# Kernel tuning notes

Hardware: AMD Instinct MI355X
Metric: run time of the kernel (lower is better)

## Reference

```python
import jax, jax.numpy as jnp
import numpy as np

N_NODES = 30000
N_EDGES = 300000
N_GRAPHS = 512
SEQ = 1000
HEADS = 10
CH = 78


def setup_inputs() -> dict:
    key = jax.random.key(0)
    ks = jax.random.split(key, 20)
    def w(k, shape, scale=0.02):
        return jax.random.normal(k, shape, jnp.float32) * scale
    x = jax.random.normal(ks[0], (N_NODES, CH), jnp.float32)
    edge_index = jax.random.randint(ks[1], (2, N_EDGES), 0, N_NODES, jnp.int32)
    # every graph gets a contiguous block of nodes (sorted batch vector)
    batch = (jnp.arange(N_NODES) * N_GRAPHS // N_NODES).astype(jnp.int32)
    target = jax.random.randint(ks[2], (N_GRAPHS, SEQ), 0, 26, jnp.int32)
    return {
        "x": x, "edge_index": edge_index, "batch": batch, "target": target,
        "W_gat": w(ks[3], (CH, HEADS * CH)),
        "att_src": w(ks[4], (HEADS, CH), 0.1),
        "att_dst": w(ks[5], (HEADS, CH), 0.1),
        "b_gat": jnp.zeros((HEADS * CH,), jnp.float32),
        "W_gcn": w(ks[6], (HEADS * CH, HEADS * CH)),
        "b_gcn": jnp.zeros((HEADS * CH,), jnp.float32),
        "W_fcg1": w(ks[7], (2 * HEADS * CH, 1500)), "b_fcg1": jnp.zeros((1500,), jnp.float32),
        "W_fcg2": w(ks[8], (1500, 128)), "b_fcg2": jnp.zeros((128,), jnp.float32),
        "emb": w(ks[9], (26, 128), 1.0),
        "W_conv": w(ks[10], (32, 1000, 8)), "b_conv": jnp.zeros((32,), jnp.float32),
        "W_fcxt": w(ks[11], (32 * 121, 128)), "b_fcxt": jnp.zeros((128,), jnp.float32),
        "W_fc1": w(ks[12], (256, 1024)), "b_fc1": jnp.zeros((1024,), jnp.float32),
        "W_fc2": w(ks[13], (1024, 512)), "b_fc2": jnp.zeros((512,), jnp.float32),
        "W_out": w(ks[14], (512, 1)), "b_out": jnp.zeros((1,), jnp.float32),
    }


def reference(x, edge_index, batch, target,
              W_gat, att_src, att_dst, b_gat, W_gcn, b_gcn,
              W_fcg1, b_fcg1, W_fcg2, b_fcg2, emb, W_conv, b_conv,
              W_fcxt, b_fcxt, W_fc1, b_fc1, W_fc2, b_fc2, W_out, b_out):
    N = x.shape[0]
    loop = jnp.arange(N, dtype=edge_index.dtype)
    src = jnp.concatenate([edge_index[0], loop])  # self-loops (PyG default)
    dst = jnp.concatenate([edge_index[1], loop])

    # ---- GATConv(78 -> 78, heads=10, concat) ----
    h = (x @ W_gat).reshape(N, HEADS, CH)           # [N,H,C]
    a_s = jnp.einsum('nhc,hc->nh', h, att_src)      # [N,H]
    a_d = jnp.einsum('nhc,hc->nh', h, att_dst)
    logits = jax.nn.leaky_relu(a_s[src] + a_d[dst], 0.2)   # [E',H]
    m = jax.ops.segment_max(logits, dst, num_segments=N)
    e = jnp.exp(logits - m[dst])
    denom = jax.ops.segment_sum(e, dst, num_segments=N)
    alpha = e / (denom[dst] + 1e-16)                # per-dst softmax
    xg = jax.ops.segment_sum(h[src] * alpha[:, :, None], dst, num_segments=N)
    xg = jax.nn.relu(xg.reshape(N, HEADS * CH) + b_gat)

    # ---- GCNConv(780 -> 780), symmetric norm with self-loops ----
    deg = jax.ops.segment_sum(jnp.ones_like(dst, dtype=xg.dtype), dst, num_segments=N)
    dinv = jax.lax.rsqrt(jnp.maximum(deg, 1.0))
    norm = dinv[src] * dinv[dst]                    # [E']
    xw = xg @ W_gcn
    xg = jax.ops.segment_sum(xw[src] * norm[:, None], dst, num_segments=N) + b_gcn
    xg = jax.nn.relu(xg)

    # ---- global max + mean pooling per graph ----
    gmax = jax.ops.segment_max(xg, batch, num_segments=N_GRAPHS)
    cnt = jax.ops.segment_sum(jnp.ones((N,), xg.dtype), batch, num_segments=N_GRAPHS)
    gmean = jax.ops.segment_sum(xg, batch, num_segments=N_GRAPHS) / cnt[:, None]
    xp = jnp.concatenate([gmax, gmean], axis=1)     # [G,1560]
    xp = jax.nn.relu(xp @ W_fcg1 + b_fcg1)          # dropout = identity (eval)
    xp = xp @ W_fcg2 + b_fcg2                       # [G,128]

    # ---- protein branch ----
    xt = emb[target]                                # [G,1000,128]
    conv = jax.lax.conv_general_dilated(
        xt, W_conv, window_strides=(1,), padding='VALID',
        dimension_numbers=('NCH', 'OIH', 'NCH'))    # [G,32,121]
    conv = conv + b_conv[None, :, None]
    xt = conv.reshape(conv.shape[0], -1) @ W_fcxt + b_fcxt  # [G,128]

    # ---- joint MLP ----
    xc = jnp.concatenate([xp, xt], axis=1)          # [G,256]
    xc = jax.nn.relu(xc @ W_fc1 + b_fc1)
    xc = jax.nn.relu(xc @ W_fc2 + b_fc2)
    return xc @ W_out + b_out                       # [G,1]
```

## Files before the change

### kernel.cpp

```cpp
#include <hip/hip_runtime.h>
#include <hip/hip_bf16.h>
#include <cstdint>
#include <cstddef>

#define N_NODES 30000
#define E0      300000
#define EPRIME  330000
#define NG      512
#define SEQL    1000
#define HEADS   10
#define CHN     78
#define HC      780
#define HP      800
#define MAXD    64

typedef __attribute__((ext_vector_type(8))) short bf16x8;
typedef __attribute__((ext_vector_type(4))) float f32x4;
typedef __attribute__((ext_vector_type(8))) unsigned short u16x8;

static __device__ __forceinline__ int src_of(const int* ei, int e){
  return (e < E0) ? ei[e] : (e - E0);
}
static __device__ __forceinline__ int dst_of(const int* ei, int e){
  return (e < E0) ? ei[E0 + e] : (e - E0);
}
static __device__ __forceinline__ unsigned short f2bf(float f){
  union { float f; unsigned u; } a; a.f = f;
  unsigned r = a.u + 0x7fff + ((a.u >> 16) & 1);
  return (unsigned short)(r >> 16);
}
static __device__ __forceinline__ float bf2f(unsigned short u){
  union { unsigned u; float f; } a; a.u = ((unsigned)u) << 16; return a.f;
}
static __device__ __forceinline__ void gl_lds16(const unsigned short* g, unsigned short* l){
  __builtin_amdgcn_global_load_lds(
      (const __attribute__((address_space(1))) void*)g,
      (__attribute__((address_space(3))) void*)l,
      16, 0, 0);
}

__global__ __launch_bounds__(256) void k_w2t(const float* __restrict__ W_conv, float* __restrict__ w2t,
                                             int* __restrict__ cnt){
  int b = blockIdx.x;
  int o = threadIdx.x >> 3, k = threadIdx.x & 7;
  w2t[(size_t)b*256 + threadIdx.x] = W_conv[(size_t)o*8000 + b*8 + k];
  int zi = b*256 + threadIdx.x;
  if (zi < N_NODES) cnt[zi] = 0;
}

static __device__ void transp_tile(const float* __restrict__ src, unsigned short* __restrict__ dst,
                                   int K, int N, int Kp, int bx, int by, int hpad){
  __shared__ float t[32][33];
  int k0 = bx*32, n0 = by*32;
  int c = threadIdx.x & 31, r = threadIdx.x >> 5;
  #pragma unroll
  for (int i=0;i<4;i++){
    int k = k0 + r + i*8;
    float v = 0.f;
    if (k < K && n0 + c < N) v = src[(size_t)k*N + n0 + c];
    t[r + i*8][c] = v;
  }
  __syncthreads();
  #pragma unroll
  for (int i=0;i<4;i++){
    int nn = n0 + r + i*8;
    int kk = k0 + c;
    if (nn < N){
      if (hpad){
        if (kk < K){
          int hh = kk/78;
          dst[(size_t)nn*Kp + hh*80 + (kk - hh*78)] = f2bf(t[c][r + i*8]);
        }
      } else {
        if (kk < Kp) dst[(size_t)nn*Kp + kk] = f2bf(t[c][r + i*8]);
      }
    }
  }
}

static __device__ void conv_body(int g, int tid, const int* __restrict__ target,
                                 const float* __restrict__ W2t, const float* __restrict__ emb,
                                 const float* __restrict__ b_conv, float* __restrict__ convf){
  int pg = tid & 7;
  __shared__ int   tgt[SEQL];
  __shared__ int   cntv[26];
  __shared__ int   startv[27];
  __shared__ int   ofs[26];
  __shared__ alignas(16) unsigned short posv[SEQL];
  __shared__ float sE[26*128 + 32];

  for (int i = tid; i < 26*128; i += 256) sE[i] = emb[i];
  if (tid < 32) sE[26*128 + tid] = 0.f;
  if (tid < 26) cntv[tid] = 0;
  const int* tg = target + g*SEQL;
  for (int i = tid; i < SEQL; i += 256) tgt[i] = tg[i];
  __syncthreads();
  for (int i = tid; i < SEQL; i += 256) atomicAdd(&cntv[tgt[i]], 1);
  __syncthreads();
  if (tid == 0){
    int s = 0;
    #pragma unroll
    for (int v = 0; v < 26; v++){ startv[v] = s; ofs[v] = s; s += cntv[v]; }
    startv[26] = s;
  }
  __syncthreads();
  for (int i = tid; i < SEQL; i += 256){
    int v = tgt[i];
    int slot = atomicAdd(&ofs[v], 1);
    posv[slot] = (unsigned short)i;
  }
  __syncthreads();

  const float* wp2 = W2t + tid;
  int p0 = pg * 16;
  int np = 121 - p0; if (np > 16) np = 16;
  int lb = (tid & 63) & 56;
  float acc[16];
  #pragma unroll
  for (int i=0;i<16;i++) acc[i]=0.f;

  for (int v = 0; v < 26; v++){
    int jb = startv[v], je = startv[v+1];
    float s = 0.f;
    for (int j = jb; j < je; j += 8){
      float w[8];
      #pragma unroll
      for (int q = 0; q < 8; q++){
        int idx = j + q;
        int p = (int)posv[(idx < je) ? idx : jb];
        float val = wp2[p << 8];
        w[q] = (idx < je) ? val : 0.f;
      }
      #pragma unroll
      for (int q = 0; q < 8; q++) s += w[q];
    }
    float u[8];
    #pragma unroll
    for (int k = 0; k < 8; k++) u[k] = __shfl(s, lb + k, 64);
    const float* ep = &sE[v*128 + p0];
    float e[24];
    #pragma unroll
    for (int i2=0;i2<24;i2+=4){
      float4 q4 = *(const float4*)(ep + i2);
      e[i2]=q4.x; e[i2+1]=q4.y; e[i2+2]=q4.z; e[i2+3]=q4.w;
    }
    #pragma unroll
    for (int pl=0; pl<16; pl++){
      acc[pl] += u[0]*e[pl]   + u[1]*e[pl+1] + u[2]*e[pl+2] + u[3]*e[pl+3]
               + u[4]*e[pl+4] + u[5]*e[pl+5] + u[6]*e[pl+6] + u[7]*e[pl+7];
    }
  }
  int o = tid >> 3;
  float bo = b_conv[o];
  for (int pl=0; pl<np; pl++)
    convf[(size_t)g*3872 + o*121 + p0 + pl] = acc[pl] + bo;
}

__global__ __launch_bounds__(256) void k_prep(
    const float* __restrict__ x, unsigned short* __restrict__ xb,
    const float* __restrict__ W_gat, unsigned short* __restrict__ wgat_t,
    const float* __restrict__ W_gcn, unsigned short* __restrict__ wgcn_t,
    const float* __restrict__ W_fcg1, unsigned short* __restrict__ wfcg1_t,
    const int* __restrict__ target, const float* __restrict__ w2t,
    const float* __restrict__ emb, const float* __restrict__ b_conv, float* __restrict__ convf,
    unsigned short* __restrict__ xwbp,
    float* __restrict__ xc, float* __restrict__ t1, float* __restrict__ t2, float* __restrict__ fg1,
    const float* __restrict__ b_fcg2, const float* __restrict__ b_fcxt,
    const float* __restrict__ b_fc1, const float* __restrict__ b_fc2,
    const float* __restrict__ b_fcg1,
    const int* __restrict__ ei, int* __restrict__ cnt, int* __restrict__ bkt)
{
  int b = blockIdx.x;
  int tid = threadIdx.x;
  if (b < 512){ conv_body(b, tid, target, w2t, emb, b_conv, convf); return; }
  b -= 512;
  if (b < 11250){
    int idx = b*256 + tid;
    if (idx < N_NODES*96){
      int n = idx/96, k = idx - n*96;
      xb[idx] = (k < CHN) ? f2bf(x[(size_t)n*CHN + k]) : 0;
    }
    return;
  }
  b -= 11250;
  if (b < 75){ transp_tile(W_gat, wgat_t, CHN, HC, 96, b%3, b/3, 0); return; }
  b -= 75;
  if (b < 625){ transp_tile(W_gcn, wgcn_t, HC, HC, HP, b%25, b/25, 1); return; }
  b -= 625;
  if (b < 2303){ transp_tile(W_fcg1, wfcg1_t, 1560, 1500, 1568, b%49, b/49, 0); return; }
  b -= 2303;
  if (b < 512){
    int g = b;
    int zi = g*256 + tid;
    if (tid < 128){
      xc[(size_t)g*256 + tid]       = b_fcg2[tid];
      xc[(size_t)g*256 + 128 + tid] = b_fcxt[tid];
    }
    for (int i = tid; i < 1024; i += 256) t1[(size_t)g*1024 + i] = b_fc1[i];
    for (int i = tid; i < 512;  i += 256) t2[(size_t)g*512  + i] = b_fc2[i];
    for (int i = tid; i < 1500; i += 256) fg1[(size_t)g*1500 + i] = b_fcg1[i];
    for (int i = tid; i < 59; i += 256){
      int n = g + i*512;
      if (n < N_NODES)
        *reinterpret_cast<unsigned long long*>(xwbp + (size_t)n*HP + HC) = 0ull;
    }
    if (zi < 7800){
      int nn = zi/10, p = zi - (zi/10)*10;
      *reinterpret_cast<unsigned*>(wgcn_t + (size_t)nn*HP + p*80 + 78) = 0u;
    }
    return;
  }
  b -= 512;
  {
    int e = b*256 + tid;
    if (e < EPRIME){
      int d = dst_of(ei, e);
      int s = src_of(ei, e);
      int slot = atomicAdd(&cnt[d], 1);
      if (slot < MAXD) bkt[d*MAXD + slot] = s;
    }
  }
}

__global__ __launch_bounds__(256) void k_mfma_bt(
    const unsigned short* __restrict__ A, const unsigned short* __restrict__ Bt,
    const float* __restrict__ bias, float* __restrict__ C, unsigned short* __restrict__ Cb,
    int M, int N, int Kp, int ldc, int relu,
    int ntc, int ntr, int ntk, int Kc, int accum, int hpad)
{
  const int total = ntc*ntr*ntk;
  const int per = (total + 7) >> 3;
  const int b = blockIdx.x;
  const int w = (b & 7)*per + (b >> 3);
  if (w >= total) return;
  const int kt = w / (ntc*ntr);
  const int r2 = w - kt*(ntc*ntr);
  const int row_t = r2 / ntc, col_t = r2 - row_t*ntc;
  const int row0 = row_t*128, col0 = col_t*128;
  const int kbeg = kt*Kc;
  const int kend = min(kbeg + Kc, Kp);

  __shared__ unsigned short As[2][128*32];
  __shared__ unsigned short Bs[2][128*32];
  const int tid = threadIdx.x;
  const int lane = tid & 63;
  const int wv = tid >> 6;
  const int wm = wv >> 1, wn = wv & 1;
  const int quad = lane >> 4, l16 = lane & 15;
  const int srow = lane >> 2;
  const int cidx = lane & 3;
  const int scol = (cidx ^ (srow & 3)) * 8;

  f32x4 acc[4][4];
  #pragma unroll
  for (int mi=0;mi<4;mi++)
    #pragma unroll
    for (int ni=0;ni<4;ni++){
      acc[mi][ni][0]=0.f; acc[mi][ni][1]=0.f; acc[mi][ni][2]=0.f; acc[mi][ni][3]=0.f;
    }

  auto stage = [&](int bsel, int kk){
    #pragma unroll
    for (int i=0;i<2;i++){
      int ch = wv*2 + i;
      int r  = ch*16 + srow;
      gl_lds16(A  + (size_t)(row0 + r)*Kp + kk + scol, &As[bsel][ch*512]);
      gl_lds16(Bt + (size_t)(col0 + r)*Kp + kk + scol, &Bs[bsel][ch*512]);
    }
  };

  const int nt = (kend - kbeg) >> 5;
  stage(0, kbeg);
  __syncthreads();
  int cur = 0;
  for (int t = 0; t < nt; ++t){
    if (t+1 < nt) stage(cur^1, kbeg + ((t+1) << 5));
    bf16x8 af[4], bfr[4];
    #pragma unroll
    for (int mi=0;mi<4;mi++)
      af[mi]  = *(const bf16x8*)(&As[cur][(wm*64 + mi*16 + l16)*32 + ((quad ^ (l16 & 3))*8)]);
    #pragma unroll
    for (int ni=0;ni<4;ni++)
      bfr[ni] = *(const bf16x8*)(&Bs[cur][(wn*64 + ni*16 + l16)*32 + ((quad ^ (l16 & 3))*8)]);
    #pragma unroll
    for (int mi=0;mi<4;mi++)
      #pragma unroll
      for (int ni=0;ni<4;ni++)
        acc[mi][ni] = __builtin_amdgcn_mfma_f32_16x16x32_bf16(af[mi], bfr[ni], acc[mi][ni], 0,0,0);
    __syncthreads();
    cur ^= 1;
  }

  #pragma unroll
  for (int mi=0;mi<4;mi++){
    #pragma unroll
    for (int rr=0;rr<4;rr++){
      int row = row0 + wm*64 + mi*16 + quad*4 + rr;
      if (row >= M) continue;
      #pragma unroll
      for (int ni=0;ni<4;ni++){
        int col = col0 + wn*64 + ni*16 + l16;
        if (col >= N) continue;
        float v = acc[mi][ni][rr];
        if (accum){
          atomicAdd(&C[(size_t)row*ldc + col], v);
        } else {
          if (bias) v += bias[col];
          if (relu) v = fmaxf(v, 0.f);
          int cs = col;
          if (hpad){ int hh = col/78; cs = hh*80 + (col - hh*78); }
          if (Cb) Cb[(size_t)row*ldc + cs] = f2bf(v);
          else    C [(size_t)row*ldc + cs] = v;
        }
      }
    }
  }
}

static __device__ void gemm_sk_body(const float* __restrict__ A, const float* __restrict__ B,
    float* __restrict__ C, int M, int N, int K, int lda, int ldb, int ldc, int Kc, int relu_a,
    int bx, int by, int bz)
{
  __shared__ float As[16][34];
  __shared__ float Bs[16][64];
  const int tid = threadIdx.x;
  const int tx = tid & 15, ty = tid >> 4;
  const int row0 = by * 32, col0 = bx * 64;
  const int kbeg = bz * Kc;
  const int kend = min(kbeg + Kc, K);
  float acc[2][4];
  #pragma unroll
  for (int i=0;i<2;i++)
    #pragma unroll
    for (int j=0;j<4;j++) acc[i][j] = 0.f;

  for (int k0 = kbeg; k0 < kend; k0 += 16){
    #pragma unroll
    for (int i=0;i<2;i++){
      int idx = tid + i*256;
      int r = idx >> 4, c = idx & 15;
      int gr = row0 + r, gc = k0 + c;
      float v = (gr < M && gc < kend) ? A[(size_t)gr*lda + gc] : 0.f;
      if (relu_a) v = fmaxf(v, 0.f);
      As[c][r] = v;
    }
    #pragma unroll
    for (int i=0;i<4;i++){
      int idx = tid + i*256;
      int r = idx >> 6, c = idx & 63;
      int gr = k0 + r, gc = col0 + c;
      Bs[r][c] = (gr < kend && gc < N) ? B[(size_t)gr*ldb + gc] : 0.f;
    }
    __syncthreads();
    #pragma unroll
    for (int kk=0; kk<16; kk++){
      float a0 = As[kk][ty*2], a1 = As[kk][ty*2+1];
      float b0 = Bs[kk][tx*4], b1 = Bs[kk][tx*4+1], b2 = Bs[kk][tx*4+2], b3 = Bs[kk][tx*4+3];
      acc[0][0]+=a0*b0; acc[0][1]+=a0*b1; acc[0][2]+=a0*b2; acc[0][3]+=a0*b3;
      acc[1][0]+=a1*b0; acc[1][1]+=a1*b1; acc[1][2]+=a1*b2; acc[1][3]+=a1*b3;
    }
    __syncthreads();
  }
  #pragma unroll
  for (int i=0;i<2;i++){
    int r = row0 + ty*2 + i;
    if (r >= M) continue;
    #pragma unroll
    for (int j=0;j<4;j++){
      int c = col0 + tx*4 + j;
      if (c < N) atomicAdd(&C[(size_t)r*ldc + c], acc[i][j]);
    }
  }
}

__global__ __launch_bounds__(256) void k_gemm_sk(const float* __restrict__ A, const float* __restrict__ B,
    float* __restrict__ C, int M, int N, int K, int lda, int ldb, int ldc, int Kc, int relu_a)
{
  gemm_sk_body(A, B, C, M, N, K, lda, ldb, ldc, Kc, relu_a,
               blockIdx.x, blockIdx.y, blockIdx.z);
}

__global__ __launch_bounds__(256) void k_gemm_dual(
    const float* __restrict__ A1, const float* __restrict__ B1, float* __restrict__ C1,
    int K1, int lda1, int ldb1, int ldc1, int Kc1, int relu1, int nz1,
    const float* __restrict__ A2, const float* __restrict__ B2, float* __restrict__ C2,
    int K2, int lda2, int ldb2, int ldc2, int Kc2, int relu2)
{
  const float *A, *B; float* C; int K, lda, ldb, ldc, Kc, relu, z;
  if ((int)blockIdx.z < nz1){
    A=A1; B=B1; C=C1; K=K1; lda=lda1; ldb=ldb1; ldc=ldc1; Kc=Kc1; relu=relu1; z=blockIdx.z;
  } else {
    A=A2; B=B2; C=C2; K=K2; lda=lda2; ldb=ldb2; ldc=ldc2; Kc=Kc2; relu=relu2; z=blockIdx.z-nz1;
  }
  gemm_sk_body(A, B, C, NG, 128, K, lda, ldb, ldc, Kc, relu, blockIdx.x, blockIdx.y, z);
}

__global__ __launch_bounds__(256) void k_attn(const unsigned short* __restrict__ hb,
    const float* __restrict__ att_src, const float* __restrict__ att_dst,
    float* __restrict__ a_s, float* __restrict__ a_d){
  __shared__ float ssrc[HC], sdst[HC];
  for (int i = threadIdx.x; i < HC; i += 256){ ssrc[i]=att_src[i]; sdst[i]=att_dst[i]; }
  __syncthreads();
  int idx = blockIdx.x*256 + threadIdx.x;
  if (idx >= N_NODES*HEADS) return;
  int n  = idx / HEADS;
  int hh = idx - n*HEADS;
  const unsigned* hp2 = (const unsigned*)(hb + (size_t)n*HP + hh*80);
  const float* as_ = ssrc + hh*CHN;
  const float* ad_ = sdst + hh*CHN;
  float s1=0.f, s2=0.f;
  #pragma unroll 13
  for (int c2=0;c2<39;c2++){
    unsigned u = hp2[c2];
    float v0 = bf2f((unsigned short)(u & 0xffffu));
    float v1 = bf2f((unsigned short)(u >> 16));
    int c = 2*c2;
    s1 += v0*as_[c] + v1*as_[c+1];
    s2 += v0*ad_[c] + v1*ad_[c+1];
  }
  a_s[idx]=s1; a_d[idx]=s2;
}

__global__ __launch_bounds__(256) void k_gat_agg(
    const unsigned short* __restrict__ hb, const float* __restrict__ a_s, const float* __restrict__ a_d,
    const float* __restrict__ b_gat, const int* __restrict__ cnt, const int* __restrict__ bkt,
    unsigned short* __restrict__ xgb, float* __restrict__ dinv)
{
  int half = threadIdx.x >> 7;
  int lt   = threadIdx.x & 127;
  int n = blockIdx.x*2 + half;
  int deg = cnt[n];
  int degc = min(deg, MAXD);
  __shared__ int   s_src[2][MAXD];
  __shared__ float s_adn[2][HEADS];
  __shared__ float s_lg[2][MAXD*HEADS];
  __shared__ float s_al[2][MAXD*HEADS];
  if (lt < HEADS) s_adn[half][lt] = a_d[(size_t)n*HEADS + lt];
  if (lt < degc)  s_src[half][lt] = bkt[n*MAXD + lt];
  __syncthreads();
  for (int idx = lt; idx < degc*HEADS; idx += 128){
    int j = idx/HEADS, t = idx - j*HEADS;
    float l = a_s[(size_t)s_src[half][j]*HEADS + t] + s_adn[half][t];
    s_lg[half][idx] = (l > 0.f) ? l : 0.2f*l;
  }
  __syncthreads();
  if (lt < HEADS){
    float m = -3.4e38f;
    for (int j=0;j<degc;j++) m = fmaxf(m, s_lg[half][j*HEADS+lt]);
    float s = 0.f;
    for (int j=0;j<degc;j++){ float e = __expf(s_lg[half][j*HEADS+lt]-m); s_al[half][j*HEADS+lt]=e; s+=e; }
    float inv = 1.f/(s + 1e-16f);
    for (int j=0;j<degc;j++) s_al[half][j*HEADS+lt] *= inv;
  }
  __syncthreads();
  if (lt < 100){
    int h = lt/10;
    int r = lt - h*10;
    int nv = (r==9) ? 6 : 8;
    int chb = h*CHN + r*8;
    const float* alp = &s_al[half][h];
    float acc[8];
    #pragma unroll
    for (int e=0;e<8;e++) acc[e]=0.f;
    auto ld = [&](int j, uint4& v, float& a){
      int s = s_src[half][j];
      a = alp[j*HEADS];
      v = *((const uint4*)(hb + (size_t)s*HP) + lt);
    };
    auto fm = [&](const uint4& v, float a){
      unsigned uu[4] = {v.x, v.y, v.z, v.w};
      #pragma unroll
      for (int e2=0;e2<4;e2++){
        acc[2*e2]   += a*bf2f((unsigned short)(uu[e2] & 0xffffu));
        acc[2*e2+1] += a*bf2f((unsigned short)(uu[e2] >> 16));
      }
    };
    int j = 0;
    for (; j+4 <= degc; j += 4){
      uint4 v0,v1,v2,v3; float a0,a1,a2,a3;
      ld(j,v0,a0); ld(j+1,v1,a1); ld(j+2,v2,a2); ld(j+3,v3,a3);
      fm(v0,a0); fm(v1,a1); fm(v2,a2); fm(v3,a3);
    }
    if (j+2 <= degc){
      uint4 v0,v1; float a0,a1;
      ld(j,v0,a0); ld(j+1,v1,a1);
      fm(v0,a0); fm(v1,a1);
      j += 2;
    }
    if (j < degc){
      uint4 v0; float a0;
      ld(j,v0,a0); fm(v0,a0);
    }
    u16x8 o;
    #pragma unroll
    for (int e=0;e<8;e++){
      float ov = (e < nv) ? fmaxf(acc[e] + b_gat[chb+e], 0.f) : 0.f;
      o[e] = f2bf(ov);
    }
    *((u16x8*)(xgb + (size_t)n*HP) + lt) = o;
  }
  if (lt == 0) dinv[n] = rsqrtf((float)deg);
}

__global__ __launch_bounds__(256) void k_gcn_agg(
    const unsigned short* __restrict__ xwb, const float* __restrict__ dinv, const float* __restrict__ b_gcn,
    const int* __restrict__ cnt, const int* __restrict__ bkt,
    unsigned short* __restrict__ xg2b)
{
  int half = threadIdx.x >> 7;
  int lt   = threadIdx.x & 127;
  int n = blockIdx.x*2 + half;
  int deg = min(cnt[n], MAXD);
  __shared__ int   s_src[2][MAXD];
  __shared__ float s_w[2][MAXD];
  if (lt < deg){
    int s = bkt[n*MAXD + lt];
    s_src[half][lt] = s;
    s_w[half][lt] = dinv[s];
  }
  __syncthreads();
  if (lt < 98){
    int ch0 = lt*8;
    float acc[8];
    #pragma unroll
    for (int e=0;e<8;e++) acc[e]=0.f;
    auto ld = [&](int j, uint4& v, float& a){
      int s = s_src[half][j];
      a = s_w[half][j];
      v = *((const uint4*)(xwb + (size_t)s*HP) + lt);
    };
    auto fm = [&](const uint4& v, float a){
      unsigned uu[4] = {v.x, v.y, v.z, v.w};
      #pragma unroll
      for (int e2=0;e2<4;e2++){
        acc[2*e2]   += a*bf2f((unsigned short)(uu[e2] & 0xffffu));
        acc[2*e2+1] += a*bf2f((unsigned short)(uu[e2] >> 16));
      }
    };
    int j = 0;
    for (; j+4 <= deg; j += 4){
      uint4 v0,v1,v2,v3; float a0,a1,a2,a3;
      ld(j,v0,a0); ld(j+1,v1,a1); ld(j+2,v2,a2); ld(j+3,v3,a3);
      fm(v0,a0); fm(v1,a1); fm(v2,a2); fm(v3,a3);
    }
    if (j+2 <= deg){
      uint4 v0,v1; float a0,a1;
      ld(j,v0,a0); ld(j+1,v1,a1);
      fm(v0,a0); fm(v1,a1);
      j += 2;
    }
    if (j < deg){
      uint4 v0; float a0;
      ld(j,v0,a0); fm(v0,a0);
    }
    float dn = dinv[n];
    ushort4 o0, o1;
    float r0 = fmaxf(dn*acc[0] + ((ch0   < HC) ? b_gcn[ch0  ] : 0.f), 0.f);
    float r1 = fmaxf(dn*acc[1] + ((ch0+1 < HC) ? b_gcn[ch0+1] : 0.f), 0.f);
    float r2 = fmaxf(dn*acc[2] + ((ch0+2 < HC) ? b_gcn[ch0+2] : 0.f), 0.f);
    float r3 = fmaxf(dn*acc[3] + ((ch0+3 < HC) ? b_gcn[ch0+3] : 0.f), 0.f);
    float r4 = fmaxf(dn*acc[4] + ((ch0+4 < HC) ? b_gcn[ch0+4] : 0.f), 0.f);
    float r5 = fmaxf(dn*acc[5] + ((ch0+5 < HC) ? b_gcn[ch0+5] : 0.f), 0.f);
    float r6 = fmaxf(dn*acc[6] + ((ch0+6 < HC) ? b_gcn[ch0+6] : 0.f), 0.f);
    float r7 = fmaxf(dn*acc[7] + ((ch0+7 < HC) ? b_gcn[ch0+7] : 0.f), 0.f);
    o0.x=f2bf(r0); o0.y=f2bf(r1); o0.z=f2bf(r2); o0.w=f2bf(r3);
    o1.x=f2bf(r4); o1.y=f2bf(r5); o1.z=f2bf(r6); o1.w=f2bf(r7);
    unsigned short* row = xg2b + (size_t)n*HC;
    *(ushort4*)(row + ch0) = o0;
    if (ch0+4 < HC) *(ushort4*)(row + ch0+4) = o1;
  }
}

__global__ __launch_bounds__(256) void k_pool(const unsigned short* __restrict__ xg2b,
                                              unsigned short* __restrict__ xpb){
  int g = blockIdx.x;
  int n0 = (N_NODES*g + NG-1) >> 9;
  int n1 = (N_NODES*(g+1) + NG-1) >> 9;
  float inv = 1.f/(float)(n1 - n0);
  int c4 = threadIdx.x;
  if (c4 < 195){
    const ushort4* x4 = (const ushort4*)xg2b;
    float m0=-3.4e38f,m1=-3.4e38f,m2=-3.4e38f,m3=-3.4e38f;
    float s0=0.f,s1=0.f,s2=0.f,s3=0.f;
    for (int n = n0; n < n1; n++){
      ushort4 v = x4[(size_t)n*195 + c4];
      float a=bf2f(v.x), b=bf2f(v.y), c=bf2f(v.z), d=bf2f(v.w);
      m0=fmaxf(m0,a); m1=fmaxf(m1,b); m2=fmaxf(m2,c); m3=fmaxf(m3,d);
      s0+=a; s1+=b; s2+=c; s3+=d;
    }
    int ch = 4*c4;
    unsigned short* row = xpb + (size_t)g*1568;
    row[ch]=f2bf(m0); row[ch+1]=f2bf(m1); row[ch+2]=f2bf(m2); row[ch+3]=f2bf(m3);
    row[HC+ch]=f2bf(s0*inv); row[HC+ch+1]=f2bf(s1*inv);
    row[HC+ch+2]=f2bf(s2*inv); row[HC+ch+3]=f2bf(s3*inv);
  }
  if (threadIdx.x < 8) xpb[(size_t)g*1568 + 1560 + threadIdx.x] = 0;
}

__global__ __launch_bounds__(64) void k_final(const float* __restrict__ t2, const float* __restrict__ W_out,
                                              const float* __restrict__ b_out, float* __restrict__ out){
  int g = blockIdx.x;
  int lane = threadIdx.x;
  const float* r = t2 + (size_t)g*512;
  float s = 0.f;
  #pragma unroll
  for (int i = lane; i < 512; i += 64) s += fmaxf(r[i], 0.f)*W_out[i];
  #pragma unroll
  for (int off=32; off; off>>=1) s += __shfl_down(s, off);
  if (lane==0) out[g] = s + b_out[0];
}

extern "C" void kernel_launch(void* const* d_in, const int* in_sizes, int n_in,
                              void* d_out, int out_size, void* d_ws, size_t ws_size,
                              hipStream_t stream) {
  const float* x      = (const float*)d_in[0];
  const int*   ei     = (const int*)  d_in[1];
  const int*   target = (const int*)  d_in[3];
  const float* W_gat  = (const float*)d_in[4];
  const float* att_src= (const float*)d_in[5];
  const float* att_dst= (const float*)d_in[6];
  const float* b_gat  = (const float*)d_in[7];
  const float* W_gcn  = (const float*)d_in[8];
  const float* b_gcn  = (const float*)d_in[9];
  const float* W_fcg1 = (const float*)d_in[10];
  const float* b_fcg1 = (const float*)d_in[11];
  const float* W_fcg2 = (const float*)d_in[12];
  const float* b_fcg2 = (const float*)d_in[13];
  const float* emb    = (const float*)d_in[14];
  const float* W_conv = (const float*)d_in[15];
  const float* b_conv = (const float*)d_in[16];
  const float* W_fcxt = (const float*)d_in[17];
  const float* b_fcxt = (const float*)d_in[18];
  const float* W_fc1  = (const float*)d_in[19];
  const float* b_fc1  = (const float*)d_in[20];
  const float* W_fc2  = (const float*)d_in[21];
  const float* b_fc2  = (const float*)d_in[22];
  const float* W_out  = (const float*)d_in[23];
  const float* b_out  = (const float*)d_in[24];
  float* out = (float*)d_out;

  char* ws = (char*)d_ws;
  size_t off = 0;
  auto alloc = [&](size_t bytes)->char*{
    char* p = ws + off;
    off += (bytes + 255) & ~(size_t)255;
    return p;
  };
  unsigned short* hb  = (unsigned short*)alloc((size_t)N_NODES*HP*2);
  unsigned short* xwb = (unsigned short*)alloc((size_t)N_NODES*HP*2);
  unsigned short* xu  = (unsigned short*)alloc((size_t)N_NODES*HP*2);
  unsigned short* xb     = (unsigned short*)alloc((size_t)N_NODES*96*2);
  unsigned short* wgat_t = (unsigned short*)alloc((size_t)HC*96*2);
  unsigned short* wgcn_t = (unsigned short*)alloc((size_t)HC*HP*2);
  unsigned short* wfcg1_t= (unsigned short*)alloc((size_t)1500*1568*2);
  unsigned short* xpb    = (unsigned short*)alloc((size_t)NG*1568*2);
  float* a_s    = (float*)alloc((size_t)N_NODES*HEADS*4);
  float* a_d    = (float*)alloc((size_t)N_NODES*HEADS*4);
  float* dinv   = (float*)alloc((size_t)N_NODES*4);
  int*   cnt    = (int*)  alloc((size_t)N_NODES*4);
  int*   bkt    = (int*)  alloc((size_t)N_NODES*MAXD*4);
  float* fg1    = (float*)alloc((size_t)NG*1500*4);
  float* convf  = (float*)alloc((size_t)NG*3872*4);
  float* xc     = (float*)alloc((size_t)NG*256*4);
  float* t1     = (float*)alloc((size_t)NG*1024*4);
  float* t2     = (float*)alloc((size_t)NG*512*4);
  float* w2t    = (float*)alloc((size_t)SEQL*256*4);

  unsigned short* xgb  = xu;
  unsigned short* xg2b = xu;

  k_w2t<<<1000, 256, 0, stream>>>(W_conv, w2t, cnt);

  k_prep<<<512+11250+75+625+2303+512+1290, 256, 0, stream>>>(
      x, xb, W_gat, wgat_t, W_gcn, wgcn_t, W_fcg1, wfcg1_t,
      target, w2t, emb, b_conv, convf, xwb,
      xc, t1, t2, fg1, b_fcg2, b_fcxt, b_fc1, b_fc2, b_fcg1,
      ei, cnt, bkt);

  auto swgrid = [](int total){ return 8 * ((total + 7) / 8); };

  k_mfma_bt<<<swgrid(7*235), 256, 0, stream>>>(xb, wgat_t, nullptr, nullptr, hb,
                                               N_NODES, HC, 96, HP, 0, 7, 235, 1, 96, 0, 1);
  k_attn<<<(N_NODES*HEADS+255)/256, 256, 0, stream>>>(hb, att_src, att_dst, a_s, a_d);
  k_gat_agg<<<N_NODES/2, 256, 0, stream>>>(hb, a_s, a_d, b_gat, cnt, bkt, xgb, dinv);

  k_mfma_bt<<<swgrid(7*235), 256, 0, stream>>>(xgb, wgcn_t, nullptr, nullptr, xwb,
                                               N_NODES, HC, HP, HP, 0, 7, 235, 1, HP, 0, 0);
  k_gcn_agg<<<N_NODES/2, 256, 0, stream>>>(xwb, dinv, b_gcn, cnt, bkt, xg2b);

  k_pool<<<NG, 256, 0, stream>>>(xg2b, xpb);
  k_mfma_bt<<<swgrid(12*4*4), 256, 0, stream>>>(xpb, wfcg1_t, nullptr, fg1, nullptr,
                                                NG, 1500, 1568, 1500, 0, 12, 4, 4, 416, 1, 0);
  k_gemm_dual<<<dim3(2, 16, 32), 256, 0, stream>>>(
      fg1,   W_fcg2, xc,       1500, 1500, 128, 256,  96, 1, 16,
      convf, W_fcxt, xc + 128, 3872, 3872, 128, 256, 248, 0);

  k_gemm_sk<<<dim3(16, 16, 2), 256, 0, stream>>>(xc, W_fc1, t1, NG, 1024, 256, 256, 1024, 1024, 128, 0);
  k_gemm_sk<<<dim3(8, 16, 4), 256, 0, stream>>>(t1, W_fc2, t2, NG, 512, 1024, 1024, 512, 512, 256, 1);
  k_final<<<NG, 64, 0, stream>>>(t2, W_out, b_out, out);
}
```

Measured before the change: 704.0 us.

## Move protein conv blocks into GAT GEMM launch and pad embedding layout

```diff
diff --git a/kernel.cpp b/kernel.cpp
--- a/kernel.cpp
+++ b/kernel.cpp
@@ -78,24 +78,27 @@
   }
 }
 
-static __device__ void conv_body(int g, int tid, const int* __restrict__ target,
+static __device__ __forceinline__ void conv_body(unsigned char* smem, int g, int tid,
+                                 const int* __restrict__ target,
                                  const float* __restrict__ W2t, const float* __restrict__ emb,
                                  const float* __restrict__ b_conv, float* __restrict__ convf){
+  float*          sE2    = (float*)smem;
+  unsigned short* posv   = (unsigned short*)(smem + 19968);
+  int*            cntv   = (int*)(smem + 21968);
+  int*            startv = cntv + 26;
+  int*            ofs    = startv + 27;
+
   int pg = tid & 7;
-  __shared__ int   tgt[SEQL];
-  __shared__ int   cntv[26];
-  __shared__ int   startv[27];
-  __shared__ int   ofs[26];
-  __shared__ alignas(16) unsigned short posv[SEQL];
-  __shared__ float sE[26*128 + 32];
-
-  for (int i = tid; i < 26*128; i += 256) sE[i] = emb[i];
-  if (tid < 32) sE[26*128 + tid] = 0.f;
+  for (int i = tid; i < 26*192; i += 256){
+    int v = i / 192, r = i - v*192;
+    int pgw = r / 24, e = r - pgw*24;
+    int col = pgw*16 + e;
+    sE2[i] = (col < 128) ? emb[v*128 + col] : 0.f;
+  }
   if (tid < 26) cntv[tid] = 0;
   const int* tg = target + g*SEQL;
-  for (int i = tid; i < SEQL; i += 256) tgt[i] = tg[i];
-  __syncthreads();
-  for (int i = tid; i < SEQL; i += 256) atomicAdd(&cntv[tgt[i]], 1);
+  __syncthreads();
+  for (int i = tid; i < SEQL; i += 256) atomicAdd(&cntv[tg[i]], 1);
   __syncthreads();
   if (tid == 0){
     int s = 0;
@@ -105,7 +108,7 @@
   }
   __syncthreads();
   for (int i = tid; i < SEQL; i += 256){
-    int v = tgt[i];
+    int v = tg[i];
     int slot = atomicAdd(&ofs[v], 1);
     posv[slot] = (unsigned short)i;
   }
@@ -137,7 +140,7 @@
     float u[8];
     #pragma unroll
     for (int k = 0; k < 8; k++) u[k] = __shfl(s, lb + k, 64);
-    const float* ep = &sE[v*128 + p0];
+    const float* ep = &sE2[v*192 + pg*24];
     float e[24];
     #pragma unroll
     for (int i2=0;i2<24;i2+=4){
@@ -161,8 +164,6 @@
     const float* __restrict__ W_gat, unsigned short* __restrict__ wgat_t,
     const float* __restrict__ W_gcn, unsigned short* __restrict__ wgcn_t,
     const float* __restrict__ W_fcg1, unsigned short* __restrict__ wfcg1_t,
-    const int* __restrict__ target, const float* __restrict__ w2t,
-    const float* __restrict__ emb, const float* __restrict__ b_conv, float* __restrict__ convf,
     unsigned short* __restrict__ xwbp,
     float* __restrict__ xc, float* __restrict__ t1, float* __restrict__ t2, float* __restrict__ fg1,
     const float* __restrict__ b_fcg2, const float* __restrict__ b_fcxt,
@@ -172,8 +173,6 @@
 {
   int b = blockIdx.x;
   int tid = threadIdx.x;
-  if (b < 512){ conv_body(b, tid, target, w2t, emb, b_conv, convf); return; }
-  b -= 512;
   if (b < 11250){
     int idx = b*256 + tid;
     if (idx < N_NODES*96){
@@ -226,11 +225,19 @@
     const unsigned short* __restrict__ A, const unsigned short* __restrict__ Bt,
     const float* __restrict__ bias, float* __restrict__ C, unsigned short* __restrict__ Cb,
     int M, int N, int Kp, int ldc, int relu,
-    int ntc, int ntr, int ntk, int Kc, int accum, int hpad)
+    int ntc, int ntr, int ntk, int Kc, int accum, int hpad,
+    int nconv, const int* __restrict__ target, const float* __restrict__ w2t,
+    const float* __restrict__ emb, const float* __restrict__ b_conv, float* __restrict__ convf)
 {
+  __shared__ alignas(16) unsigned char smem[32768];
+  const int tid = threadIdx.x;
+  if ((int)blockIdx.x < nconv){
+    conv_body(smem, blockIdx.x, tid, target, w2t, emb, b_conv, convf);
+    return;
+  }
   const int total = ntc*ntr*ntk;
   const int per = (total + 7) >> 3;
-  const int b = blockIdx.x;
+  const int b = blockIdx.x - nconv;
   const int w = (b & 7)*per + (b >> 3);
   if (w >= total) return;
   const int kt = w / (ntc*ntr);
@@ -240,9 +247,8 @@
   const int kbeg = kt*Kc;
   const int kend = min(kbeg + Kc, Kp);
 
-  __shared__ unsigned short As[2][128*32];
-  __shared__ unsigned short Bs[2][128*32];
-  const int tid = threadIdx.x;
+  unsigned short* As = (unsigned short*)smem;
+  unsigned short* Bs = (unsigned short*)(smem + 16384);
   const int lane = tid & 63;
   const int wv = tid >> 6;
   const int wm = wv >> 1, wn = wv & 1;
@@ -264,8 +270,8 @@
     for (int i=0;i<2;i++){
       int ch = wv*2 + i;
       int r  = ch*16 + srow;
-      gl_lds16(A  + (size_t)(row0 + r)*Kp + kk + scol, &As[bsel][ch*512]);
-      gl_lds16(Bt + (size_t)(col0 + r)*Kp + kk + scol, &Bs[bsel][ch*512]);
+      gl_lds16(A  + (size_t)(row0 + r)*Kp + kk + scol, &As[bsel*4096 + ch*512]);
+      gl_lds16(Bt + (size_t)(col0 + r)*Kp + kk + scol, &Bs[bsel*4096 + ch*512]);
     }
   };
 
@@ -278,10 +284,10 @@
     bf16x8 af[4], bfr[4];
     #pragma unroll
     for (int mi=0;mi<4;mi++)
-      af[mi]  = *(const bf16x8*)(&As[cur][(wm*64 + mi*16 + l16)*32 + ((quad ^ (l16 & 3))*8)]);
+      af[mi]  = *(const bf16x8*)(&As[cur*4096 + (wm*64 + mi*16 + l16)*32 + ((quad ^ (l16 & 3))*8)]);
     #pragma unroll
     for (int ni=0;ni<4;ni++)
-      bfr[ni] = *(const bf16x8*)(&Bs[cur][(wn*64 + ni*16 + l16)*32 + ((quad ^ (l16 & 3))*8)]);
+      bfr[ni] = *(const bf16x8*)(&Bs[cur*4096 + (wn*64 + ni*16 + l16)*32 + ((quad ^ (l16 & 3))*8)]);
     #pragma unroll
     for (int mi=0;mi<4;mi++)
       #pragma unroll
@@ -671,26 +677,28 @@
 
   k_w2t<<<1000, 256, 0, stream>>>(W_conv, w2t, cnt);
 
-  k_prep<<<512+11250+75+625+2303+512+1290, 256, 0, stream>>>(
-      x, xb, W_gat, wgat_t, W_gcn, wgcn_t, W_fcg1, wfcg1_t,
-      target, w2t, emb, b_conv, convf, xwb,
+  k_prep<<<11250+75+625+2303+512+1290, 256, 0, stream>>>(
+      x, xb, W_gat, wgat_t, W_gcn, wgcn_t, W_fcg1, wfcg1_t, xwb,
       xc, t1, t2, fg1, b_fcg2, b_fcxt, b_fc1, b_fc2, b_fcg1,
       ei, cnt, bkt);
 
   auto swgrid = [](int total){ return 8 * ((total + 7) / 8); };
 
-  k_mfma_bt<<<swgrid(7*235), 256, 0, stream>>>(xb, wgat_t, nullptr, nullptr, hb,
-                                               N_NODES, HC, 96, HP, 0, 7, 235, 1, 96, 0, 1);
+  k_mfma_bt<<<512 + swgrid(7*235), 256, 0, stream>>>(xb, wgat_t, nullptr, nullptr, hb,
+                                               N_NODES, HC, 96, HP, 0, 7, 235, 1, 96, 0, 1,
+                                               512, target, w2t, emb, b_conv, convf);
   k_attn<<<(N_NODES*HEADS+255)/256, 256, 0, stream>>>(hb, att_src, att_dst, a_s, a_d);
   k_gat_agg<<<N_NODES/2, 256, 0, stream>>>(hb, a_s, a_d, b_gat, cnt, bkt, xgb, dinv);
 
   k_mfma_bt<<<swgrid(7*235), 256, 0, stream>>>(xgb, wgcn_t, nullptr, nullptr, xwb,
-                                               N_NODES, HC, HP, HP, 0, 7, 235, 1, HP, 0, 0);
+                                               N_NODES, HC, HP, HP, 0, 7, 235, 1, HP, 0, 0,
+                                               0, nullptr, nullptr, nullptr, nullptr, nullptr);
   k_gcn_agg<<<N_NODES/2, 256, 0, stream>>>(xwb, dinv, b_gcn, cnt, bkt, xg2b);
 
   k_pool<<<NG, 256, 0, stream>>>(xg2b, xpb);
   k_mfma_bt<<<swgrid(12*4*4), 256, 0, stream>>>(xpb, wfcg1_t, nullptr, fg1, nullptr,
-                                                NG, 1500, 1568, 1500, 0, 12, 4, 4, 416, 1, 0);
+                                                NG, 1500, 1568, 1500, 0, 12, 4, 4, 416, 1, 0,
+                                                0, nullptr, nullptr, nullptr, nullptr, nullptr);
   k_gemm_dual<<<dim3(2, 16, 32), 256, 0, stream>>>(
       fg1,   W_fcg2, xc,       1500, 1500, 128, 256,  96, 1, 16,
       convf, W_fcxt, xc + 128, 3872, 3872, 128, 256, 248, 0);
```

Measured after the change: 692.4 us, median of 3. About the same (-1.7%).

## Split protein conv across four blocks per graph with atomic accumulation

Applied to the files above, without the earlier changes.

```diff
diff --git a/kernel.cpp b/kernel.cpp
--- a/kernel.cpp
+++ b/kernel.cpp
@@ -40,12 +40,17 @@
 }
 
 __global__ __launch_bounds__(256) void k_w2t(const float* __restrict__ W_conv, float* __restrict__ w2t,
-                                             int* __restrict__ cnt){
+                                             int* __restrict__ cnt,
+                                             const float* __restrict__ b_conv, float* __restrict__ convf){
   int b = blockIdx.x;
   int o = threadIdx.x >> 3, k = threadIdx.x & 7;
   w2t[(size_t)b*256 + threadIdx.x] = W_conv[(size_t)o*8000 + b*8 + k];
   int zi = b*256 + threadIdx.x;
   if (zi < N_NODES) cnt[zi] = 0;
+  for (size_t i = (size_t)b*256 + threadIdx.x; i < (size_t)NG*3872; i += 256000){
+    int r = (int)(i % 3872);
+    convf[i] = b_conv[r/121];
+  }
 }
 
 static __device__ void transp_tile(const float* __restrict__ src, unsigned short* __restrict__ dst,
@@ -78,24 +83,30 @@
   }
 }
 
-static __device__ void conv_body(int g, int tid, const int* __restrict__ target,
+static __device__ void conv_body(int b, int tid, const int* __restrict__ target,
                                  const float* __restrict__ W2t, const float* __restrict__ emb,
-                                 const float* __restrict__ b_conv, float* __restrict__ convf){
+                                 float* __restrict__ convf){
+  const int g = b >> 2, part = b & 3;
+  const int vlo = (part==0)?0:(part==1)?7:(part==2)?13:20;
+  const int vhi = (part==0)?7:(part==1)?13:(part==2)?20:26;
+  __shared__ float sEg[7*192];
+  __shared__ alignas(16) unsigned short posv[1008];
+  __shared__ int cntv[26];
+  __shared__ int startv[27];
+  __shared__ int ofs[26];
+
   int pg = tid & 7;
-  __shared__ int   tgt[SEQL];
-  __shared__ int   cntv[26];
-  __shared__ int   startv[27];
-  __shared__ int   ofs[26];
-  __shared__ alignas(16) unsigned short posv[SEQL];
-  __shared__ float sE[26*128 + 32];
-
-  for (int i = tid; i < 26*128; i += 256) sE[i] = emb[i];
-  if (tid < 32) sE[26*128 + tid] = 0.f;
+  for (int i = tid; i < (vhi-vlo)*192; i += 256){
+    int vv = i/192, r = i - vv*192;
+    int pgw = r/24, e = r - pgw*24;
+    int col = pgw*16 + e;
+    sEg[i] = (col < 128) ? emb[(vlo+vv)*128 + col] : 0.f;
+  }
   if (tid < 26) cntv[tid] = 0;
+  if (tid < 8) posv[1000 + tid] = 0;
   const int* tg = target + g*SEQL;
-  for (int i = tid; i < SEQL; i += 256) tgt[i] = tg[i];
-  __syncthreads();
-  for (int i = tid; i < SEQL; i += 256) atomicAdd(&cntv[tgt[i]], 1);
+  __syncthreads();
+  for (int i = tid; i < SEQL; i += 256) atomicAdd(&cntv[tg[i]], 1);
   __syncthreads();
   if (tid == 0){
     int s = 0;
@@ -105,7 +116,7 @@
   }
   __syncthreads();
   for (int i = tid; i < SEQL; i += 256){
-    int v = tgt[i];
+    int v = tg[i];
     int slot = atomicAdd(&ofs[v], 1);
     posv[slot] = (unsigned short)i;
   }
@@ -119,25 +130,24 @@
   #pragma unroll
   for (int i=0;i<16;i++) acc[i]=0.f;
 
-  for (int v = 0; v < 26; v++){
+  for (int v = vlo; v < vhi; v++){
     int jb = startv[v], je = startv[v+1];
     float s = 0.f;
-    for (int j = jb; j < je; j += 8){
+    for (int j = jb & ~7; j < je; j += 8){
+      u16x8 p8 = *(const u16x8*)&posv[j];
       float w[8];
       #pragma unroll
       for (int q = 0; q < 8; q++){
         int idx = j + q;
-        int p = (int)posv[(idx < je) ? idx : jb];
-        float val = wp2[p << 8];
-        w[q] = (idx < je) ? val : 0.f;
+        float val = wp2[(int)p8[q] << 8];
+        w[q] = (idx >= jb && idx < je) ? val : 0.f;
       }
-      #pragma unroll
-      for (int q = 0; q < 8; q++) s += w[q];
+      s += ((w[0]+w[1]) + (w[2]+w[3])) + ((w[4]+w[5]) + (w[6]+w[7]));
     }
     float u[8];
     #pragma unroll
     for (int k = 0; k < 8; k++) u[k] = __shfl(s, lb + k, 64);
-    const float* ep = &sE[v*128 + p0];
+    const float* ep = &sEg[(v - vlo)*192 + pg*24];
     float e[24];
     #pragma unroll
     for (int i2=0;i2<24;i2+=4){
@@ -151,9 +161,8 @@
     }
   }
   int o = tid >> 3;
-  float bo = b_conv[o];
-  for (int pl=0; pl<np; pl++)
-    convf[(size_t)g*3872 + o*121 + p0 + pl] = acc[pl] + bo;
+  float* outp = convf + (size_t)g*3872 + o*121 + p0;
+  for (int pl=0; pl<np; pl++) atomicAdd(&outp[pl], acc[pl]);
 }
 
 __global__ __launch_bounds__(256) void k_prep(
@@ -162,7 +171,7 @@
     const float* __restrict__ W_gcn, unsigned short* __restrict__ wgcn_t,
     const float* __restrict__ W_fcg1, unsigned short* __restrict__ wfcg1_t,
     const int* __restrict__ target, const float* __restrict__ w2t,
-    const float* __restrict__ emb, const float* __restrict__ b_conv, float* __restrict__ convf,
+    const float* __restrict__ emb, float* __restrict__ convf,
     unsigned short* __restrict__ xwbp,
     float* __restrict__ xc, float* __restrict__ t1, float* __restrict__ t2, float* __restrict__ fg1,
     const float* __restrict__ b_fcg2, const float* __restrict__ b_fcxt,
@@ -172,8 +181,8 @@
 {
   int b = blockIdx.x;
   int tid = threadIdx.x;
-  if (b < 512){ conv_body(b, tid, target, w2t, emb, b_conv, convf); return; }
-  b -= 512;
+  if (b < 2048){ conv_body(b, tid, target, w2t, emb, convf); return; }
+  b -= 2048;
   if (b < 11250){
     int idx = b*256 + tid;
     if (idx < N_NODES*96){
@@ -669,11 +678,11 @@
   unsigned short* xgb  = xu;
   unsigned short* xg2b = xu;
 
-  k_w2t<<<1000, 256, 0, stream>>>(W_conv, w2t, cnt);
-
-  k_prep<<<512+11250+75+625+2303+512+1290, 256, 0, stream>>>(
+  k_w2t<<<1000, 256, 0, stream>>>(W_conv, w2t, cnt, b_conv, convf);
+
+  k_prep<<<2048+11250+75+625+2303+512+1290, 256, 0, stream>>>(
       x, xb, W_gat, wgat_t, W_gcn, wgcn_t, W_fcg1, wfcg1_t,
-      target, w2t, emb, b_conv, convf, xwb,
+      target, w2t, emb, convf, xwb,
       xc, t1, t2, fg1, b_fcg2, b_fcxt, b_fc1, b_fc2, b_fcg1,
       ei, cnt, bkt);
 
```

Result: slower. 1.080 ms (+53.4%).
